# Kernel tuning notes

Hardware: AMD Instinct MI355X
Metric: run time of the kernel (lower is better)

## Reference

```python
import jax, jax.numpy as jnp
import numpy as np

H = 16  # n_heads

def setup_inputs() -> dict:
    key = jax.random.key(0)
    ks = jax.random.split(key, 11)
    B, L, D = 2, 2048, 1024
    w = 1.0 / np.sqrt(D).astype(np.float32)
    return {
        "query": jax.random.normal(ks[0], (B, L, D), jnp.float32),
        "key":   jax.random.normal(ks[1], (B, L, D), jnp.float32),
        "value": jax.random.normal(ks[2], (B, L, D), jnp.float32),
        "Wq": jax.random.normal(ks[3], (D, D), jnp.float32) * w,
        "bq": jax.random.normal(ks[4], (D,), jnp.float32) * 0.01,
        "Wk": jax.random.normal(ks[5], (D, D), jnp.float32) * w,
        "bk": jax.random.normal(ks[6], (D,), jnp.float32) * 0.01,
        "Wv": jax.random.normal(ks[7], (D, D), jnp.float32) * w,
        "bv": jax.random.normal(ks[8], (D,), jnp.float32) * 0.01,
        "Wo": jax.random.normal(ks[9], (D, D), jnp.float32) * w,
        "bo": jax.random.normal(ks[10], (D,), jnp.float32) * 0.01,
        "masksize": 256,
    }

def reference(query, key, value, Wq, bq, Wk, bk, Wv, bv, Wo, bo, masksize):
    B, L, D = query.shape
    d_k = D // H
    scale = 1.0 / np.sqrt(d_k).astype(np.float32)

    def proj(x, W, b):
        # nn.Linear: x @ W.T + b, then [B,L,H,d_k] -> [B,H,L,d_k]
        return (x @ W.T + b).reshape(B, L, H, d_k).transpose(0, 2, 1, 3)

    q = proj(query, Wq, bq)
    k = proj(key, Wk, bk)
    v = proj(value, Wv, bv)

    # Sliding-window float mask (faithful to original: a 0/1 FLOAT tensor is
    # passed as attn_mask to SDPA, so it is ADDED to scores, not -inf-masked).
    half = masksize // 2
    i = jnp.arange(L)[:, None]
    j = jnp.arange(L)[None, :]
    band = (jnp.abs(i - j) <= half).astype(q.dtype)  # [L, L]

    scores = jnp.einsum('bhqd,bhkd->bhqk', q, k) * scale + band  # [B,H,L,L]
    attn = jax.nn.softmax(scores, axis=-1)
    out = jnp.einsum('bhqk,bhkd->bhqd', attn, v)  # [B,H,L,d_k]
    out = out.transpose(0, 2, 1, 3).reshape(B, L, D)
    return out @ Wo.T + bo
```

## Files before the change

kernel.cpp:

```cpp
#include <hip/hip_runtime.h>
#include <hip/hip_bf16.h>

#define Hh 16
#define Ll 2048
#define Dd 1024
#define DK 64
#define Mm 4096
#define Kk 1024
#define Nn 1024

typedef short bf16x8 __attribute__((ext_vector_type(8)));
typedef float f32x4 __attribute__((ext_vector_type(4)));

static __device__ __forceinline__ unsigned short f2bf(float f) {
    union { __hip_bfloat16 b; unsigned short u; } cv;
    cv.b = __float2bfloat16(f);
    return cv.u;
}

static __device__ __forceinline__ unsigned packtr(float a, float b) {
    return __builtin_amdgcn_perm(__builtin_bit_cast(unsigned, b),
                                 __builtin_bit_cast(unsigned, a), 0x07060302u);
}

static __device__ __forceinline__ float fexp2(float x) {
    return __builtin_amdgcn_exp2f(x);
}

static __device__ __forceinline__ void glds16(const ushort* g, ushort* l) {
    __builtin_amdgcn_global_load_lds((const __attribute__((address_space(1))) unsigned int*)g,
                                     (__attribute__((address_space(3))) unsigned int*)l,
                                     16, 0, 0);
}

__global__ __launch_bounds__(256) void cast_all(
    const float* __restrict__ q, const float* __restrict__ k, const float* __restrict__ v,
    const float* __restrict__ wq, const float* __restrict__ wk, const float* __restrict__ wv,
    const float* __restrict__ wo,
    ushort* __restrict__ qb, ushort* __restrict__ kb, ushort* __restrict__ vb,
    ushort* __restrict__ wqb, ushort* __restrict__ wkb, ushort* __restrict__ wvb,
    ushort* __restrict__ wob) {
    const int bx = blockIdx.x;
    const float4* s; ushort4* d; int base;
    if      (bx <  4096) { s = (const float4*)q;  d = (ushort4*)qb;  base = 0; }
    else if (bx <  8192) { s = (const float4*)k;  d = (ushort4*)kb;  base = 4096; }
    else if (bx < 12288) { s = (const float4*)v;  d = (ushort4*)vb;  base = 8192; }
    else if (bx < 13312) { s = (const float4*)wq; d = (ushort4*)wqb; base = 12288; }
    else if (bx < 14336) { s = (const float4*)wk; d = (ushort4*)wkb; base = 13312; }
    else if (bx < 15360) { s = (const float4*)wv; d = (ushort4*)wvb; base = 14336; }
    else                 { s = (const float4*)wo; d = (ushort4*)wob; base = 15360; }
    const int i = (bx - base) * 256 + threadIdx.x;
    float4 vv = s[i];
    ushort4 o;
    o.x = f2bf(vv.x); o.y = f2bf(vv.y); o.z = f2bf(vv.z); o.w = f2bf(vv.w);
    d[i] = o;
}

__global__ __launch_bounds__(256) void gemm_qkv(
    const ushort* __restrict__ A0, const ushort* __restrict__ A1, const ushort* __restrict__ A2,
    const ushort* __restrict__ W0, const ushort* __restrict__ W1, const ushort* __restrict__ W2,
    const float* __restrict__ b0, const float* __restrict__ b1, const float* __restrict__ b2,
    ushort* __restrict__ O0, ushort* __restrict__ O1, ushort* __restrict__ OVt) {
    __shared__ __align__(16) ushort SM[2 * 128 * 32];
    ushort* As = SM;
    ushort* Bs = SM + 4096;

    const int fl = blockIdx.x;
    const int xcd = fl & 7, bcoli = (fl >> 3) & 7, slot = fl >> 6;
    const int g = slot * 8 + xcd;
    const int z = g >> 5;
    const int browi = g & 31;

    const ushort* A = (z == 0) ? A0 : (z == 1) ? A1 : A2;
    const ushort* W = (z == 0) ? W0 : (z == 1) ? W1 : W2;
    const float* bias = (z == 0) ? b0 : (z == 1) ? b1 : b2;

    const int t = threadIdx.x;
    const int wave = t >> 6, lane = t & 63;
    const int quad = lane >> 4, l15 = lane & 15;
    const int brow = browi * 128, bcol = bcoli * 128;
    const int wr = (wave >> 1) * 64, wc = (wave & 1) * 64;
    const int gr = wave * 16 + (lane >> 2);
    const int gc = (lane & 3) * 8;

    f32x4 acc[4][4] = {};

    for (int k0 = 0; k0 < Kk; k0 += 32) {
        __syncthreads();
        glds16(A + (size_t)(brow + gr) * Kk + k0 + gc,      As + wave * 512);
        glds16(A + (size_t)(brow + 64 + gr) * Kk + k0 + gc, As + 2048 + wave * 512);
        glds16(W + (size_t)(bcol + gr) * Kk + k0 + gc,      Bs + wave * 512);
        glds16(W + (size_t)(bcol + 64 + gr) * Kk + k0 + gc, Bs + 2048 + wave * 512);
        __syncthreads();

        bf16x8 af[4], bfr[4];
#pragma unroll
        for (int i = 0; i < 4; i++)
            af[i] = *(const bf16x8*)(As + (wr + i * 16 + l15) * 32 + quad * 8);
#pragma unroll
        for (int j = 0; j < 4; j++)
            bfr[j] = *(const bf16x8*)(Bs + (wc + j * 16 + l15) * 32 + quad * 8);
#pragma unroll
        for (int i = 0; i < 4; i++)
#pragma unroll
            for (int j = 0; j < 4; j++)
                acc[i][j] = __builtin_amdgcn_mfma_f32_16x16x32_bf16(af[i], bfr[j], acc[i][j], 0, 0, 0);
    }

    if (z < 2) {
        ushort* Out = (z == 0) ? O0 : O1;
        const float oscl = (z == 0) ? 0.18033688f : 1.0f;
        const int b = brow >> 11;
        const int lbase = (brow & 2047) + wr;
        const int h = (bcol + wc) >> 6;
        ushort* T = SM + wave * 1280;
        __syncthreads();
#pragma unroll
        for (int i = 0; i < 4; i++) {
#pragma unroll
            for (int j = 0; j < 4; j++) {
                const float bv = bias[bcol + wc + j * 16 + l15];
#pragma unroll
                for (int r = 0; r < 4; r++)
                    T[(quad * 4 + r) * 80 + j * 16 + l15] = f2bf((acc[i][j][r] + bv) * oscl);
            }
            const int r8 = lane >> 3, c8 = lane & 7;
#pragma unroll
            for (int pass = 0; pass < 2; pass++) {
                const uint4 val = *(const uint4*)(T + (pass * 8 + r8) * 80 + c8 * 8);
                const int l = lbase + i * 16 + pass * 8 + r8;
                *(uint4*)(Out + ((size_t)(b * Hh + h) * Ll + l) * DK + c8 * 8) = val;
            }
        }
    } else {
        ushort* T = SM;
        const int b = brow >> 11;
        const int lbase = brow & 2047;
        const int npr = (wave & 1) * 16 + l15;
#pragma unroll
        for (int j = 0; j < 4; j++) {
            __syncthreads();
            const float bv = bias[bcol + wc + j * 16 + l15];
#pragma unroll
            for (int i = 0; i < 4; i++)
#pragma unroll
                for (int r = 0; r < 4; r++) {
                    const int m = wr + i * 16 + quad * 4 + r;
                    T[npr * 136 + m] = f2bf(acc[i][j][r] + bv);
                }
            __syncthreads();
#pragma unroll
            for (int cc = 0; cc < 2; cc++) {
                const int idx = t + cc * 256;
                const int ni = idx >> 4;
                const int ms = idx & 15;
                const int n = bcol + (ni >> 4) * 64 + j * 16 + (ni & 15);
                const int hh = n >> 6, dk = n & 63;
                uint4 val = *(const uint4*)(T + ni * 136 + ms * 8);
                *(uint4*)(OVt + ((size_t)(b * Hh + hh) * DK + dk) * Ll + lbase + ms * 8) = val;
            }
        }
    }
}

__global__ __launch_bounds__(256) void attn_kernel(const ushort* __restrict__ Q,
                                                   const ushort* __restrict__ Kp,
                                                   const ushort* __restrict__ Vt,
                                                   ushort* __restrict__ Oout,
                                                   const int* __restrict__ masksize) {
    __shared__ __align__(16) ushort SM[32768];
    const int t = threadIdx.x;
    const int wave = t >> 6, lane = t & 63;
    const int quad = lane >> 4, l15 = lane & 15;
    const int bx = blockIdx.x;
    const int bh = bx & 31, qc = bx >> 5;
    const int q0w = qc * 128 + wave * 32;
    const int half = masksize[0] >> 1;
    const unsigned wid = (unsigned)(2 * half);

    const ushort* Qb = Q + (size_t)bh * (Ll * DK);
    const ushort* Kb = Kp + (size_t)bh * (Ll * DK);
    const ushort* Vb = Vt + (size_t)bh * (DK * Ll);

    const bf16x8 qA0 = *(const bf16x8*)(Qb + (size_t)(q0w + l15) * DK + quad * 8);
    const bf16x8 qA1 = *(const bf16x8*)(Qb + (size_t)(q0w + l15) * DK + 32 + quad * 8);
    const bf16x8 qB0 = *(const bf16x8*)(Qb + (size_t)(q0w + 16 + l15) * DK + quad * 8);
    const bf16x8 qB1 = *(const bf16x8*)(Qb + (size_t)(q0w + 16 + l15) * DK + 32 + quad * 8);

    const float C2IN  = (1.0f - 24.0f) * 1.44269504088896f;
    const float C2OUT = -24.0f * 1.44269504088896f;
    const float E1 = 2.718281828f;

    bf16x8 onesf;
#pragma unroll
    for (int j = 0; j < 8; j++) onesf[j] = (short)0x3F80;

    f32x4 OA[4] = {}, OB[4] = {};
    f32x4 SA = {}, SB = {};

    const int krow = lane >> 2;
    const int kcol8 = (((lane & 3) ^ ((lane >> 3) & 3)) * 8);
    const int qsw8 = (quad ^ ((l15 >> 1) & 3)) * 8;
    const int vdl = lane >> 4;
    const int vg0 = 2 * (lane & 15);

#define STAGE_KV(KT, BUF)                                                                  \
    do {                                                                                   \
        ushort* Ksb_ = SM + (BUF) * 8192;                                                  \
        ushort* Vsb_ = SM + 16384 + (BUF) * 8192;                                          \
        if (wave < 2) {                                                                    \
            const int cbase_ = wave * 4;                                                   \
            _Pragma("unroll")                                                              \
            for (int c_ = 0; c_ < 4; c_++)                                                 \
                _Pragma("unroll")                                                          \
                for (int pan_ = 0; pan_ < 2; pan_++)                                       \
                    glds16(Kb + (size_t)((KT) + (cbase_ + c_) * 16 + krow) * DK            \
                               + pan_ * 32 + kcol8,                                        \
                           Ksb_ + (pan_ * 128 + (cbase_ + c_) * 16) * 32);                 \
        } else {                                                                           \
            const int sb_ = (wave - 2) * 8;                                                \
            _Pragma("unroll")                                                              \
            for (int i_ = 0; i_ < 8; i_++) {                                               \
                const int sidx_ = sb_ + i_;                                                \
                const int d_ = sidx_ * 4 + vdl;                                            \
                const int g0_ = vg0 ^ (d_ & 30);                                           \
                glds16(Vb + (size_t)d_ * Ll + (KT) + g0_ * 4, Vsb_ + sidx_ * 512);         \
            }                                                                              \
        }                                                                                  \
    } while (0)

    STAGE_KV(0, 0);
    int cur = 0;

    for (int it = 0; it < 16; ++it) {
        const int kt = it * 128;
        __syncthreads();
        if (it < 15) STAGE_KV(kt + 128, cur ^ 1);

        const ushort* Ksb = SM + cur * 8192;
        const ushort* Vsb = SM + 16384 + cur * 8192;

        const int qlo = q0w, qhi = q0w + 31;
        const bool allout = (kt + 127 < qlo - half) || (kt > qhi + half);
        const bool allin  = (kt >= qhi - half) && (kt + 127 <= qlo + half);
        const bool uniform = allin || allout;
        const float cinit = allin ? C2IN : C2OUT;
        f32x4 cvec = {cinit, cinit, cinit, cinit};

#pragma unroll
        for (int s = 0; s < 4; s++) {
            const bf16x8 kf00 = *(const bf16x8*)(Ksb + ((2 * s) * 16 + l15) * 32 + qsw8);
            const bf16x8 kf01 = *(const bf16x8*)(Ksb + 4096 + ((2 * s) * 16 + l15) * 32 + qsw8);
            const bf16x8 kf10 = *(const bf16x8*)(Ksb + ((2 * s + 1) * 16 + l15) * 32 + qsw8);
            const bf16x8 kf11 = *(const bf16x8*)(Ksb + 4096 + ((2 * s + 1) * 16 + l15) * 32 + qsw8);
            f32x4 zA0 = __builtin_amdgcn_mfma_f32_16x16x32_bf16(kf00, qA0, cvec, 0, 0, 0);
            zA0 = __builtin_amdgcn_mfma_f32_16x16x32_bf16(kf01, qA1, zA0, 0, 0, 0);
            f32x4 zA1 = __builtin_amdgcn_mfma_f32_16x16x32_bf16(kf10, qA0, cvec, 0, 0, 0);
            zA1 = __builtin_amdgcn_mfma_f32_16x16x32_bf16(kf11, qA1, zA1, 0, 0, 0);
            f32x4 zB0 = __builtin_amdgcn_mfma_f32_16x16x32_bf16(kf00, qB0, cvec, 0, 0, 0);
            zB0 = __builtin_amdgcn_mfma_f32_16x16x32_bf16(kf01, qB1, zB0, 0, 0, 0);
            f32x4 zB1 = __builtin_amdgcn_mfma_f32_16x16x32_bf16(kf10, qB0, cvec, 0, 0, 0);
            zB1 = __builtin_amdgcn_mfma_f32_16x16x32_bf16(kf11, qB1, zB1, 0, 0, 0);

            float pA[8], pB[8];
            if (uniform) {
#pragma unroll
                for (int g = 0; g < 2; g++)
#pragma unroll
                    for (int r = 0; r < 4; r++) {
                        pA[g * 4 + r] = fexp2(g ? zA1[r] : zA0[r]);
                        pB[g * 4 + r] = fexp2(g ? zB1[r] : zB0[r]);
                    }
            } else {
                const int kb = kt + s * 32 + quad * 4 + half;
#pragma unroll
                for (int g = 0; g < 2; g++)
#pragma unroll
                    for (int r = 0; r < 4; r++) {
                        const unsigned ttA = (unsigned)(kb + g * 16 + r - (q0w + l15));
                        const unsigned ttB = (unsigned)(kb + g * 16 + r - (q0w + 16 + l15));
                        pA[g * 4 + r] = fexp2(g ? zA1[r] : zA0[r]) * (ttA <= wid ? E1 : 1.0f);
                        pB[g * 4 + r] = fexp2(g ? zB1[r] : zB0[r]) * (ttB <= wid ? E1 : 1.0f);
                    }
            }

            bf16x8 pfA, pfB;
            ((unsigned*)&pfA)[0] = packtr(pA[0], pA[1]);
            ((unsigned*)&pfA)[1] = packtr(pA[2], pA[3]);
            ((unsigned*)&pfA)[2] = packtr(pA[4], pA[5]);
            ((unsigned*)&pfA)[3] = packtr(pA[6], pA[7]);
            ((unsigned*)&pfB)[0] = packtr(pB[0], pB[1]);
            ((unsigned*)&pfB)[1] = packtr(pB[2], pB[3]);
            ((unsigned*)&pfB)[2] = packtr(pB[4], pB[5]);
            ((unsigned*)&pfB)[3] = packtr(pB[6], pB[7]);

            SA = __builtin_amdgcn_mfma_f32_16x16x32_bf16(pfA, onesf, SA, 0, 0, 0);
            SB = __builtin_amdgcn_mfma_f32_16x16x32_bf16(pfB, onesf, SB, 0, 0, 0);

#pragma unroll
            for (int i = 0; i < 4; i++) {
                const int d = i * 16 + l15;
                const int x4 = (d & 30) * 4;
                const int bi = d * 128;
                const ushort4 v1 = *(const ushort4*)(Vsb + bi + (((s * 8 + quad) * 4) ^ x4));
                const ushort4 v2 = *(const ushort4*)(Vsb + bi + (((s * 8 + 4 + quad) * 4) ^ x4));
                bf16x8 vc;
                *(ushort4*)&vc = v1;
                *((ushort4*)&vc + 1) = v2;
                OA[i] = __builtin_amdgcn_mfma_f32_16x16x32_bf16(pfA, vc, OA[i], 0, 0, 0);
                OB[i] = __builtin_amdgcn_mfma_f32_16x16x32_bf16(pfB, vc, OB[i], 0, 0, 0);
            }
        }
        cur ^= 1;
    }
#undef STAGE_KV

    float liA[4], liB[4];
#pragma unroll
    for (int r = 0; r < 4; r++) {
        liA[r] = 1.0f / SA[r];
        liB[r] = 1.0f / SB[r];
    }

    const int b = bh >> 4, h = bh & 15;
#pragma unroll
    for (int i = 0; i < 4; i++)
#pragma unroll
        for (int r = 0; r < 4; r++) {
            const int qa = q0w + quad * 4 + r;
            Oout[((size_t)b * Ll + qa) * Dd + h * DK + i * 16 + l15] = f2bf(OA[i][r] * liA[r]);
            Oout[((size_t)b * Ll + qa + 16) * Dd + h * DK + i * 16 + l15] = f2bf(OB[i][r] * liB[r]);
        }
}

__global__ __launch_bounds__(256) void gemm_o(const ushort* __restrict__ A,
                                              const ushort* __restrict__ W,
                                              const float* __restrict__ bias,
                                              float* __restrict__ Out) {
    __shared__ __align__(16) ushort As[64 * 32];
    __shared__ __align__(16) ushort Bs[128 * 32];
    const int fl = blockIdx.x;
    const int xcd = fl & 7, bcoli = (fl >> 3) & 7, slot = fl >> 6;
    const int g = slot * 8 + xcd;
    const int t = threadIdx.x;
    const int wave = t >> 6, lane = t & 63;
    const int quad = lane >> 4, l15 = lane & 15;
    const int brow = g * 64, bcol = bcoli * 128;
    const int wr = (wave >> 1) * 32, wc = (wave & 1) * 64;
    const int gr = wave * 16 + (lane >> 2);
    const int gc = (lane & 3) * 8;

    f32x4 acc[2][4] = {};

    for (int k0 = 0; k0 < Kk; k0 += 32) {
        __syncthreads();
        glds16(A + (size_t)(brow + gr) * Kk + k0 + gc,      As + wave * 512);
        glds16(W + (size_t)(bcol + gr) * Kk + k0 + gc,      Bs + wave * 512);
        glds16(W + (size_t)(bcol + 64 + gr) * Kk + k0 + gc, Bs + 2048 + wave * 512);
        __syncthreads();

        bf16x8 af[2], bfr[4];
#pragma unroll
        for (int i = 0; i < 2; i++)
            af[i] = *(const bf16x8*)(As + (wr + i * 16 + l15) * 32 + quad * 8);
#pragma unroll
        for (int j = 0; j < 4; j++)
            bfr[j] = *(const bf16x8*)(Bs + (wc + j * 16 + l15) * 32 + quad * 8);
#pragma unroll
        for (int i = 0; i < 2; i++)
#pragma unroll
            for (int j = 0; j < 4; j++)
                acc[i][j] = __builtin_amdgcn_mfma_f32_16x16x32_bf16(af[i], bfr[j], acc[i][j], 0, 0, 0);
    }

#pragma unroll
    for (int i = 0; i < 2; i++)
#pragma unroll
        for (int j = 0; j < 4; j++) {
            const int n = bcol + wc + j * 16 + l15;
            const float bv = bias[n];
#pragma unroll
            for (int r = 0; r < 4; r++) {
                const int m = brow + wr + i * 16 + quad * 4 + r;
                Out[(size_t)m * Nn + n] = acc[i][j][r] + bv;
            }
        }
}

extern "C" void kernel_launch(void* const* d_in, const int* in_sizes, int n_in,
                              void* d_out, int out_size, void* d_ws, size_t ws_size,
                              hipStream_t stream) {
    const float* query = (const float*)d_in[0];
    const float* key   = (const float*)d_in[1];
    const float* value = (const float*)d_in[2];
    const float* Wq = (const float*)d_in[3];
    const float* bq = (const float*)d_in[4];
    const float* Wk = (const float*)d_in[5];
    const float* bk = (const float*)d_in[6];
    const float* Wv = (const float*)d_in[7];
    const float* bv = (const float*)d_in[8];
    const float* Wo = (const float*)d_in[9];
    const float* bo = (const float*)d_in[10];
    const int* masksize = (const int*)d_in[11];

    char* ws = (char*)d_ws;
    const size_t MB = 1024 * 1024;
    ushort* qb  = (ushort*)(ws + 0 * MB);
    ushort* kbf = (ushort*)(ws + 8 * MB);
    ushort* vbf = (ushort*)(ws + 16 * MB);
    ushort* wqb = (ushort*)(ws + 24 * MB);
    ushort* wkb = (ushort*)(ws + 26 * MB);
    ushort* wvb = (ushort*)(ws + 28 * MB);
    ushort* wob = (ushort*)(ws + 30 * MB);
    ushort* Qp  = (ushort*)(ws + 32 * MB);
    ushort* Kp  = (ushort*)(ws + 40 * MB);
    ushort* Vt  = (ushort*)(ws + 48 * MB);
    ushort* AO  = (ushort*)(ws + 56 * MB);

    cast_all<<<16384, 256, 0, stream>>>(query, key, value, Wq, Wk, Wv, Wo,
                                        qb, kbf, vbf, wqb, wkb, wvb, wob);

    gemm_qkv<<<768, 256, 0, stream>>>(qb, kbf, vbf,
                                      wqb, wkb, wvb,
                                      bq, bk, bv,
                                      Qp, Kp, Vt);

    attn_kernel<<<512, 256, 0, stream>>>(Qp, Kp, Vt, AO, masksize);

    gemm_o<<<512, 256, 0, stream>>>(AO, wob, bo, (float*)d_out);
}
```

Before: 218.5 us.

## Split attention KV loop into two independent streams with separate accumulators

Each block now processes two interleaved 64-key tiles per iteration, one from the first half of the sequence and one from the second, each with its own output and row-sum accumulators that are combined at the end. The intent is to expose more independent MFMA and exp work for latency hiding, and launch bounds now request two blocks per CU. This doubles accumulator registers, so the occupancy hint may force spills. Any iteration where either tile is non-uniform falls back to the masked path for both tiles.

```diff
diff --git a/kernel.cpp b/kernel.cpp
--- a/kernel.cpp
+++ b/kernel.cpp
@@ -163,11 +163,11 @@
     }
 }
 
-__global__ __launch_bounds__(256) void attn_kernel(const ushort* __restrict__ Q,
-                                                   const ushort* __restrict__ Kp,
-                                                   const ushort* __restrict__ Vt,
-                                                   ushort* __restrict__ Oout,
-                                                   const int* __restrict__ masksize) {
+__global__ __launch_bounds__(256, 2) void attn_kernel(const ushort* __restrict__ Q,
+                                                      const ushort* __restrict__ Kp,
+                                                      const ushort* __restrict__ Vt,
+                                                      ushort* __restrict__ Oout,
+                                                      const int* __restrict__ masksize) {
     __shared__ __align__(16) ushort SM[32768];
     const int t = threadIdx.x;
     const int wave = t >> 6, lane = t & 63;
@@ -195,131 +195,141 @@
 #pragma unroll
     for (int j = 0; j < 8; j++) onesf[j] = (short)0x3F80;
 
-    f32x4 OA[4] = {}, OB[4] = {};
-    f32x4 SA = {}, SB = {};
+    f32x4 OA0[4] = {}, OB0[4] = {}, OA1[4] = {}, OB1[4] = {};
+    f32x4 SA0 = {}, SB0 = {}, SA1 = {}, SB1 = {};
 
     const int krow = lane >> 2;
     const int kcol8 = (((lane & 3) ^ ((lane >> 3) & 3)) * 8);
     const int qsw8 = (quad ^ ((l15 >> 1) & 3)) * 8;
-    const int vdl = lane >> 4;
-    const int vg0 = 2 * (lane & 15);
-
-#define STAGE_KV(KT, BUF)                                                                  \
+    const int vd8 = lane >> 3;
+    const int vgp = 2 * (lane & 7);
+
+#define STAGE_J(J, BUF)                                                                    \
     do {                                                                                   \
-        ushort* Ksb_ = SM + (BUF) * 8192;                                                  \
-        ushort* Vsb_ = SM + 16384 + (BUF) * 8192;                                          \
+        const int kt0_ = (J) * 64, kt1_ = 1024 + (J) * 64;                                 \
         if (wave < 2) {                                                                    \
-            const int cbase_ = wave * 4;                                                   \
+            const int ktk_ = (wave == 0) ? kt0_ : kt1_;                                    \
+            ushort* dst_ = SM + wave * 8192 + (BUF) * 4096;                                \
             _Pragma("unroll")                                                              \
             for (int c_ = 0; c_ < 4; c_++)                                                 \
                 _Pragma("unroll")                                                          \
                 for (int pan_ = 0; pan_ < 2; pan_++)                                       \
-                    glds16(Kb + (size_t)((KT) + (cbase_ + c_) * 16 + krow) * DK            \
-                               + pan_ * 32 + kcol8,                                        \
-                           Ksb_ + (pan_ * 128 + (cbase_ + c_) * 16) * 32);                 \
+                    glds16(Kb + (size_t)(ktk_ + c_ * 16 + krow) * DK + pan_ * 32 + kcol8,  \
+                           dst_ + pan_ * 2048 + c_ * 512);                                 \
         } else {                                                                           \
-            const int sb_ = (wave - 2) * 8;                                                \
+            const int ktv_ = (wave == 2) ? kt0_ : kt1_;                                    \
+            ushort* dst_ = SM + 16384 + (wave - 2) * 8192 + (BUF) * 4096;                  \
             _Pragma("unroll")                                                              \
-            for (int i_ = 0; i_ < 8; i_++) {                                               \
-                const int sidx_ = sb_ + i_;                                                \
-                const int d_ = sidx_ * 4 + vdl;                                            \
-                const int g0_ = vg0 ^ (d_ & 30);                                           \
-                glds16(Vb + (size_t)d_ * Ll + (KT) + g0_ * 4, Vsb_ + sidx_ * 512);         \
+            for (int s_ = 0; s_ < 8; s_++) {                                               \
+                const int d_ = s_ * 8 + vd8;                                               \
+                glds16(Vb + (size_t)d_ * Ll + ktv_ + ((vgp ^ (d_ & 14)) * 4),              \
+                       dst_ + s_ * 512);                                                   \
             }                                                                              \
         }                                                                                  \
     } while (0)
 
-    STAGE_KV(0, 0);
+#define STREAM_BODY(KB, VB, KT, CV, OAx, OBx, SAx, SBx, UNIF)                              \
+    _Pragma("unroll")                                                                      \
+    for (int s = 0; s < 2; s++) {                                                          \
+        const bf16x8 kf00 = *(const bf16x8*)((KB) + ((2 * s) * 16 + l15) * 32 + qsw8);     \
+        const bf16x8 kf01 = *(const bf16x8*)((KB) + 2048 + ((2 * s) * 16 + l15) * 32 + qsw8); \
+        const bf16x8 kf10 = *(const bf16x8*)((KB) + ((2 * s + 1) * 16 + l15) * 32 + qsw8); \
+        const bf16x8 kf11 = *(const bf16x8*)((KB) + 2048 + ((2 * s + 1) * 16 + l15) * 32 + qsw8); \
+        f32x4 zA0 = __builtin_amdgcn_mfma_f32_16x16x32_bf16(kf00, qA0, (CV), 0, 0, 0);     \
+        zA0 = __builtin_amdgcn_mfma_f32_16x16x32_bf16(kf01, qA1, zA0, 0, 0, 0);            \
+        f32x4 zA1 = __builtin_amdgcn_mfma_f32_16x16x32_bf16(kf10, qA0, (CV), 0, 0, 0);     \
+        zA1 = __builtin_amdgcn_mfma_f32_16x16x32_bf16(kf11, qA1, zA1, 0, 0, 0);            \
+        f32x4 zB0 = __builtin_amdgcn_mfma_f32_16x16x32_bf16(kf00, qB0, (CV), 0, 0, 0);     \
+        zB0 = __builtin_amdgcn_mfma_f32_16x16x32_bf16(kf01, qB1, zB0, 0, 0, 0);            \
+        f32x4 zB1 = __builtin_amdgcn_mfma_f32_16x16x32_bf16(kf10, qB0, (CV), 0, 0, 0);     \
+        zB1 = __builtin_amdgcn_mfma_f32_16x16x32_bf16(kf11, qB1, zB1, 0, 0, 0);            \
+        float pA[8], pB[8];                                                                \
+        if (UNIF) {                                                                        \
+            _Pragma("unroll")                                                              \
+            for (int g = 0; g < 2; g++)                                                    \
+                _Pragma("unroll")                                                          \
+                for (int r = 0; r < 4; r++) {                                              \
+                    pA[g * 4 + r] = fexp2(g ? zA1[r] : zA0[r]);                            \
+                    pB[g * 4 + r] = fexp2(g ? zB1[r] : zB0[r]);                            \
+                }                                                                          \
+        } else {                                                                           \
+            const int kb = (KT) + s * 32 + quad * 4 + half;                                \
+            _Pragma("unroll")                                                              \
+            for (int g = 0; g < 2; g++)                                                    \
+                _Pragma("unroll")                                                          \
+                for (int r = 0; r < 4; r++) {                                              \
+                    const unsigned ttA = (unsigned)(kb + g * 16 + r - (q0w + l15));        \
+                    const unsigned ttB = (unsigned)(kb + g * 16 + r - (q0w + 16 + l15));   \
+                    pA[g * 4 + r] = fexp2(g ? zA1[r] : zA0[r]) * (ttA <= wid ? E1 : 1.0f); \
+                    pB[g * 4 + r] = fexp2(g ? zB1[r] : zB0[r]) * (ttB <= wid ? E1 : 1.0f); \
+                }                                                                          \
+        }                                                                                  \
+        bf16x8 pfA, pfB;                                                                   \
+        ((unsigned*)&pfA)[0] = packtr(pA[0], pA[1]);                                       \
+        ((unsigned*)&pfA)[1] = packtr(pA[2], pA[3]);                                       \
+        ((unsigned*)&pfA)[2] = packtr(pA[4], pA[5]);                                       \
+        ((unsigned*)&pfA)[3] = packtr(pA[6], pA[7]);                                       \
+        ((unsigned*)&pfB)[0] = packtr(pB[0], pB[1]);                                       \
+        ((unsigned*)&pfB)[1] = packtr(pB[2], pB[3]);                                       \
+        ((unsigned*)&pfB)[2] = packtr(pB[4], pB[5]);                                       \
+        ((unsigned*)&pfB)[3] = packtr(pB[6], pB[7]);                                       \
+        SAx = __builtin_amdgcn_mfma_f32_16x16x32_bf16(pfA, onesf, SAx, 0, 0, 0);           \
+        SBx = __builtin_amdgcn_mfma_f32_16x16x32_bf16(pfB, onesf, SBx, 0, 0, 0);           \
+        _Pragma("unroll")                                                                  \
+        for (int i = 0; i < 4; i++) {                                                      \
+            const int bi = (i * 16 + l15) * 64;                                            \
+            const int x14 = l15 & 14;                                                      \
+            const ushort4 v1 = *(const ushort4*)((VB) + bi + (((s * 8 + quad) ^ x14) * 4)); \
+            const ushort4 v2 = *(const ushort4*)((VB) + bi + (((s * 8 + 4 + quad) ^ x14) * 4)); \
+            bf16x8 vc;                                                                     \
+            *(ushort4*)&vc = v1;                                                           \
+            *((ushort4*)&vc + 1) = v2;                                                     \
+            OAx[i] = __builtin_amdgcn_mfma_f32_16x16x32_bf16(pfA, vc, OAx[i], 0, 0, 0);    \
+            OBx[i] = __builtin_amdgcn_mfma_f32_16x16x32_bf16(pfB, vc, OBx[i], 0, 0, 0);    \
+        }                                                                                  \
+    }
+
+    STAGE_J(0, 0);
     int cur = 0;
-
-    for (int it = 0; it < 16; ++it) {
-        const int kt = it * 128;
-        __syncthreads();
-        if (it < 15) STAGE_KV(kt + 128, cur ^ 1);
-
-        const ushort* Ksb = SM + cur * 8192;
-        const ushort* Vsb = SM + 16384 + cur * 8192;
-
-        const int qlo = q0w, qhi = q0w + 31;
-        const bool allout = (kt + 127 < qlo - half) || (kt > qhi + half);
-        const bool allin  = (kt >= qhi - half) && (kt + 127 <= qlo + half);
-        const bool uniform = allin || allout;
-        const float cinit = allin ? C2IN : C2OUT;
-        f32x4 cvec = {cinit, cinit, cinit, cinit};
-
-#pragma unroll
-        for (int s = 0; s < 4; s++) {
-            const bf16x8 kf00 = *(const bf16x8*)(Ksb + ((2 * s) * 16 + l15) * 32 + qsw8);
-            const bf16x8 kf01 = *(const bf16x8*)(Ksb + 4096 + ((2 * s) * 16 + l15) * 32 + qsw8);
-            const bf16x8 kf10 = *(const bf16x8*)(Ksb + ((2 * s + 1) * 16 + l15) * 32 + qsw8);
-            const bf16x8 kf11 = *(const bf16x8*)(Ksb + 4096 + ((2 * s + 1) * 16 + l15) * 32 + qsw8);
-            f32x4 zA0 = __builtin_amdgcn_mfma_f32_16x16x32_bf16(kf00, qA0, cvec, 0, 0, 0);
-            zA0 = __builtin_amdgcn_mfma_f32_16x16x32_bf16(kf01, qA1, zA0, 0, 0, 0);
-            f32x4 zA1 = __builtin_amdgcn_mfma_f32_16x16x32_bf16(kf10, qA0, cvec, 0, 0, 0);
-            zA1 = __builtin_amdgcn_mfma_f32_16x16x32_bf16(kf11, qA1, zA1, 0, 0, 0);
-            f32x4 zB0 = __builtin_amdgcn_mfma_f32_16x16x32_bf16(kf00, qB0, cvec, 0, 0, 0);
-            zB0 = __builtin_amdgcn_mfma_f32_16x16x32_bf16(kf01, qB1, zB0, 0, 0, 0);
-            f32x4 zB1 = __builtin_amdgcn_mfma_f32_16x16x32_bf16(kf10, qB0, cvec, 0, 0, 0);
-            zB1 = __builtin_amdgcn_mfma_f32_16x16x32_bf16(kf11, qB1, zB1, 0, 0, 0);
-
-            float pA[8], pB[8];
-            if (uniform) {
-#pragma unroll
-                for (int g = 0; g < 2; g++)
-#pragma unroll
-                    for (int r = 0; r < 4; r++) {
-                        pA[g * 4 + r] = fexp2(g ? zA1[r] : zA0[r]);
-                        pB[g * 4 + r] = fexp2(g ? zB1[r] : zB0[r]);
-                    }
-            } else {
-                const int kb = kt + s * 32 + quad * 4 + half;
-#pragma unroll
-                for (int g = 0; g < 2; g++)
-#pragma unroll
-                    for (int r = 0; r < 4; r++) {
-                        const unsigned ttA = (unsigned)(kb + g * 16 + r - (q0w + l15));
-                        const unsigned ttB = (unsigned)(kb + g * 16 + r - (q0w + 16 + l15));
-                        pA[g * 4 + r] = fexp2(g ? zA1[r] : zA0[r]) * (ttA <= wid ? E1 : 1.0f);
-                        pB[g * 4 + r] = fexp2(g ? zB1[r] : zB0[r]) * (ttB <= wid ? E1 : 1.0f);
-                    }
-            }
-
-            bf16x8 pfA, pfB;
-            ((unsigned*)&pfA)[0] = packtr(pA[0], pA[1]);
-            ((unsigned*)&pfA)[1] = packtr(pA[2], pA[3]);
-            ((unsigned*)&pfA)[2] = packtr(pA[4], pA[5]);
-            ((unsigned*)&pfA)[3] = packtr(pA[6], pA[7]);
-            ((unsigned*)&pfB)[0] = packtr(pB[0], pB[1]);
-            ((unsigned*)&pfB)[1] = packtr(pB[2], pB[3]);
-            ((unsigned*)&pfB)[2] = packtr(pB[4], pB[5]);
-            ((unsigned*)&pfB)[3] = packtr(pB[6], pB[7]);
-
-            SA = __builtin_amdgcn_mfma_f32_16x16x32_bf16(pfA, onesf, SA, 0, 0, 0);
-            SB = __builtin_amdgcn_mfma_f32_16x16x32_bf16(pfB, onesf, SB, 0, 0, 0);
-
-#pragma unroll
-            for (int i = 0; i < 4; i++) {
-                const int d = i * 16 + l15;
-                const int x4 = (d & 30) * 4;
-                const int bi = d * 128;
-                const ushort4 v1 = *(const ushort4*)(Vsb + bi + (((s * 8 + quad) * 4) ^ x4));
-                const ushort4 v2 = *(const ushort4*)(Vsb + bi + (((s * 8 + 4 + quad) * 4) ^ x4));
-                bf16x8 vc;
-                *(ushort4*)&vc = v1;
-                *((ushort4*)&vc + 1) = v2;
-                OA[i] = __builtin_amdgcn_mfma_f32_16x16x32_bf16(pfA, vc, OA[i], 0, 0, 0);
-                OB[i] = __builtin_amdgcn_mfma_f32_16x16x32_bf16(pfB, vc, OB[i], 0, 0, 0);
-            }
+    const int qlo = q0w, qhi = q0w + 31;
+
+    for (int j = 0; j < 16; ++j) {
+        const int kt0 = j * 64, kt1 = 1024 + j * 64;
+        __syncthreads();
+        if (j < 15) STAGE_J(j + 1, cur ^ 1);
+
+        const ushort* K0b = SM + cur * 4096;
+        const ushort* K1b = SM + 8192 + cur * 4096;
+        const ushort* V0b = SM + 16384 + cur * 4096;
+        const ushort* V1b = SM + 24576 + cur * 4096;
+
+        const bool allout0 = (kt0 + 63 < qlo - half) || (kt0 > qhi + half);
+        const bool allin0  = (kt0 >= qhi - half) && (kt0 + 63 <= qlo + half);
+        const bool allout1 = (kt1 + 63 < qlo - half) || (kt1 > qhi + half);
+        const bool allin1  = (kt1 >= qhi - half) && (kt1 + 63 <= qlo + half);
+
+        if ((allin0 || allout0) && (allin1 || allout1)) {
+            const float c0 = allin0 ? C2IN : C2OUT;
+            const float c1 = allin1 ? C2IN : C2OUT;
+            const f32x4 cv0 = {c0, c0, c0, c0};
+            const f32x4 cv1 = {c1, c1, c1, c1};
+            STREAM_BODY(K0b, V0b, kt0, cv0, OA0, OB0, SA0, SB0, 1);
+            STREAM_BODY(K1b, V1b, kt1, cv1, OA1, OB1, SA1, SB1, 1);
+        } else {
+            const f32x4 cvo = {C2OUT, C2OUT, C2OUT, C2OUT};
+            STREAM_BODY(K0b, V0b, kt0, cvo, OA0, OB0, SA0, SB0, 0);
+            STREAM_BODY(K1b, V1b, kt1, cvo, OA1, OB1, SA1, SB1, 0);
         }
         cur ^= 1;
     }
-#undef STAGE_KV
+#undef STAGE_J
+#undef STREAM_BODY
 
     float liA[4], liB[4];
 #pragma unroll
     for (int r = 0; r < 4; r++) {
-        liA[r] = 1.0f / SA[r];
-        liB[r] = 1.0f / SB[r];
+        liA[r] = 1.0f / (SA0[r] + SA1[r]);
+        liB[r] = 1.0f / (SB0[r] + SB1[r]);
     }
 
     const int b = bh >> 4, h = bh & 15;
@@ -328,8 +338,10 @@
 #pragma unroll
         for (int r = 0; r < 4; r++) {
             const int qa = q0w + quad * 4 + r;
-            Oout[((size_t)b * Ll + qa) * Dd + h * DK + i * 16 + l15] = f2bf(OA[i][r] * liA[r]);
-            Oout[((size_t)b * Ll + qa + 16) * Dd + h * DK + i * 16 + l15] = f2bf(OB[i][r] * liB[r]);
+            Oout[((size_t)b * Ll + qa) * Dd + h * DK + i * 16 + l15] =
+                f2bf((OA0[i][r] + OA1[i][r]) * liA[r]);
+            Oout[((size_t)b * Ll + qa + 16) * Dd + h * DK + i * 16 + l15] =
+                f2bf((OB0[i][r] + OB1[i][r]) * liB[r]);
         }
 }
 
```

Result: no change. 219.1 us (+0.3%).
